# Kernel optimization log

Measured on AMD Instinct MI355X. Metric: run time of the kernel, lower is better.

## Reference

```python
import jax, jax.numpy as jnp
import numpy as np

B, F, D, U = 4096, 32, 64, 256


def setup_inputs() -> dict:
    key = jax.random.key(0)
    k1, k2, k3, k4 = jax.random.split(key, 4)
    embeds = jax.random.normal(k1, (B, F, D), dtype=jnp.float32)
    # glorot-ish scaling for the learned weights
    linear_w = jax.random.normal(k2, (F * D, U), dtype=jnp.float32) * (2.0 / (F * D + U)) ** 0.5
    inner_w = jax.random.normal(k3, (U, F), dtype=jnp.float32) * (2.0 / (U + F)) ** 0.5
    outer_w = jax.random.normal(k4, (U, D, D), dtype=jnp.float32) * (2.0 / (2 * D)) ** 0.5
    return {"embeds": embeds, "linear_w": linear_w, "inner_w": inner_w, "outer_w": outer_w}


def reference(embeds, linear_w, inner_w, outer_w):
    b = embeds.shape[0]
    # linear signal lz: flatten fields and project -> [B, U]
    lz = embeds.reshape(b, -1) @ linear_w
    # inner products: per unit u, delta_u = sum_f w_{u,f} * e_f  -> [B, U, D];
    # lp_inner[b,u] = ||delta_u||^2 (collapses the per-unit TF loop into one einsum)
    delta = jnp.einsum('bfd,uf->bud', embeds, inner_w)
    lp_inner = jnp.sum(jnp.square(delta), axis=2)  # [B, U]
    # outer products: product = fs fs^T with fs = sum_f e_f; lp_outer[b,u] = <product_b, W_u>
    fs = jnp.sum(embeds, axis=1)  # [B, D]
    lp_outer = jnp.einsum('bi,bj,uij->bu', fs, fs, outer_w)  # [B, U]
    return jnp.concatenate([lz, lp_inner, lp_outer], axis=1)  # [B, 3U]
```

## Files before the change

### kernel.cpp

```cpp
#include <hip/hip_runtime.h>
#include <hip/hip_bf16.h>


#define KA 3072
#define KW 7168

typedef __attribute__((ext_vector_type(8))) short short8v;
typedef __attribute__((ext_vector_type(4))) float f32x4;

#define GLOAD(src, dst) __builtin_amdgcn_global_load_lds( \
    (const __attribute__((address_space(1))) void*)(src), \
    (__attribute__((address_space(3))) void*)(dst), 16, 0, 0)

static __device__ __forceinline__ short f2bf(float f) {
    union { float f; unsigned u; } v; v.f = f;
    unsigned r = v.u + 0x7fffu + ((v.u >> 16) & 1u);
    return (short)(r >> 16);
}
static __device__ __forceinline__ float bf2f(short s) {
    union { unsigned u; float f; } v; v.u = ((unsigned)(unsigned short)s) << 16;
    return v.f;
}
static __device__ __forceinline__ int cvtpk(float lo, float hi) {
    int r;
    asm("v_cvt_pk_bf16_f32 %0, %1, %2" : "=v"(r) : "v"(lo), "v"(hi));
    return r;
}

__global__ __launch_bounds__(256) void prep(const float* __restrict__ embeds,
                                            const float* __restrict__ lw,
                                            const float* __restrict__ iw,
                                            const float* __restrict__ ow,
                                            short* __restrict__ A,
                                            short* __restrict__ FS,
                                            short* __restrict__ Wt) {
    __shared__ float se[2048];
    __shared__ short sebf[2048];
    int t = threadIdx.x;

    if (blockIdx.x < 4096) {
        int b = blockIdx.x;
        const float* e = embeds + (size_t)b * 2048;
        short* arow = A + (size_t)b * KA;

        float4 v0 = ((const float4*)e)[t * 2];
        float4 v1 = ((const float4*)e)[t * 2 + 1];
        ((float4*)se)[t * 2] = v0;
        ((float4*)se)[t * 2 + 1] = v1;
        short8v sb;
        sb[0] = f2bf(v0.x); sb[1] = f2bf(v0.y); sb[2] = f2bf(v0.z); sb[3] = f2bf(v0.w);
        sb[4] = f2bf(v1.x); sb[5] = f2bf(v1.y); sb[6] = f2bf(v1.z); sb[7] = f2bf(v1.w);
        ((short8v*)sebf)[t] = sb;
        *(short8v*)&arow[t * 8] = sb;

        __syncthreads();
        if (t < 64) {
            float s = 0.f;
            #pragma unroll
            for (int f = 0; f < 32; ++f) s += se[f * 64 + t];
            FS[(size_t)b * 64 + t] = f2bf(s);
        }

        int wid = t >> 6, lane = t & 63;
        int tm = wid >> 1, tn = wid & 1;
        int lr = lane & 15, lk = (lane >> 4) * 8;
        f32x4 g = {0.f, 0.f, 0.f, 0.f};
        #pragma unroll
        for (int ks = 0; ks < 2; ++ks) {
            short8v a  = *(const short8v*)&sebf[(tm * 16 + lr) * 64 + ks * 32 + lk];
            short8v bb = *(const short8v*)&sebf[(tn * 16 + lr) * 64 + ks * 32 + lk];
            g = __builtin_amdgcn_mfma_f32_16x16x32_bf16(a, bb, g, 0, 0, 0);
        }
        #pragma unroll
        for (int r = 0; r < 4; ++r) {
            int grow = tm * 16 + (lane >> 4) * 4 + r;
            int gcol = tn * 16 + lr;
            arow[2048 + grow * 32 + gcol] = f2bf(g[r]);
        }
    } else {
        int u = blockIdx.x - 4096;
        short* w = Wt + (size_t)u * KW;

        for (int k = t; k < 2048; k += 256) w[k] = f2bf(lw[(size_t)k * 256 + u]);

        if (t < 32) se[t] = iw[u * 32 + t];
        __syncthreads();
        for (int idx = t; idx < 1024; idx += 256)
            w[2048 + idx] = f2bf(se[idx >> 5] * se[idx & 31]);

        const float* owu = ow + (size_t)u * 4096;
        for (int i = t; i < 512; i += 256) {
            float4 a = ((const float4*)owu)[i * 2];
            float4 b = ((const float4*)owu)[i * 2 + 1];
            short8v s;
            s[0] = f2bf(a.x); s[1] = f2bf(a.y); s[2] = f2bf(a.z); s[3] = f2bf(a.w);
            s[4] = f2bf(b.x); s[5] = f2bf(b.y); s[6] = f2bf(b.z); s[7] = f2bf(b.w);
            *(short8v*)&w[3072 + i * 8] = s;
        }
    }
}

__global__ __launch_bounds__(256) void gemm_tile(const short* __restrict__ A,
                                                 const short* __restrict__ Wt,
                                                 const short* __restrict__ FS,
                                                 float* __restrict__ out) {
    __shared__ short As[2][8192];
    __shared__ short Bs[2][4096];

    int id = blockIdx.x;
    int seg, loc;
    if (id < 128)      { seg = 0; loc = id; }
    else if (id < 256) { seg = 2; loc = id - 128; }
    else               { seg = 1; loc = id - 256; }
    int mt = loc >> 2, nt = loc & 3;
    const int nk = (seg == 0) ? 32 : (seg == 1) ? 16 : 64;
    int brow = mt * 128, bcol = nt * 64;
    int akoff = (seg == 1) ? 2048 : 0;
    int boff  = (seg == 0) ? 0 : (seg == 1) ? 2048 : 3072;

    int t = threadIdx.x, w = t >> 6, lane = t & 63;
    int lr = lane & 15, hi = lane >> 4;
    int srow = t >> 3;
    int soct = (t & 7) ^ (srow & 7);

    const short* Asrc = A  + (size_t)(brow + srow) * KA + akoff + soct * 8;
    const short* Bsrc = Wt + (size_t)(bcol + srow) * KW + boff  + soct * 8;
    const short* Fsrc = FS + (size_t)(brow + srow) * 64 + soct * 8;

    auto stageA = [&](int p, int kt) {
        #pragma unroll
        for (int i = 0; i < 4; ++i)
            GLOAD(Asrc + (size_t)i * 32 * KA + kt * 64, &As[p][i * 2048 + t * 8]);
    };
    auto stageB = [&](int p, int kt) {
        #pragma unroll
        for (int i = 0; i < 2; ++i)
            GLOAD(Bsrc + (size_t)i * 32 * KW + kt * 64, &Bs[p][i * 2048 + t * 8]);
    };

    f32x4 acc[2][4];
    #pragma unroll
    for (int m = 0; m < 2; ++m)
        #pragma unroll
        for (int n = 0; n < 4; ++n) acc[m][n] = (f32x4){0.f, 0.f, 0.f, 0.f};

    if (seg == 2) {
        #pragma unroll
        for (int i = 0; i < 4; ++i)
            GLOAD(Fsrc + (size_t)i * 32 * 64, &As[0][i * 2048 + t * 8]);
        stageB(0, 0);
    } else {
        stageA(0, 0); stageB(0, 0);
    }
    __syncthreads();

    if (seg != 2) {
        for (int kt = 0; kt < nk; ++kt) {
            int cur = kt & 1;
            if (kt + 1 < nk) { stageA(cur ^ 1, kt + 1); stageB(cur ^ 1, kt + 1); }
            #pragma unroll
            for (int ks = 0; ks < 2; ++ks) {
                int oct = ((ks * 4 + hi) ^ (lr & 7)) * 8;
                short8v a[2], b[4];
                #pragma unroll
                for (int m = 0; m < 2; ++m)
                    a[m] = *(const short8v*)&As[cur][(w * 32 + m * 16 + lr) * 64 + oct];
                #pragma unroll
                for (int n = 0; n < 4; ++n)
                    b[n] = *(const short8v*)&Bs[cur][(n * 16 + lr) * 64 + oct];
                #pragma unroll
                for (int m = 0; m < 2; ++m)
                    #pragma unroll
                    for (int n = 0; n < 4; ++n)
                        acc[m][n] = __builtin_amdgcn_mfma_f32_16x16x32_bf16(a[m], b[n], acc[m][n], 0, 0, 0);
            }
            __syncthreads();
        }
    } else {
        float fj[2][2][8];
        #pragma unroll
        for (int m = 0; m < 2; ++m)
            #pragma unroll
            for (int ks = 0; ks < 2; ++ks) {
                int oct = ((ks * 4 + hi) ^ (lr & 7)) * 8;
                short8v v = *(const short8v*)&As[0][(w * 32 + m * 16 + lr) * 64 + oct];
                #pragma unroll
                for (int e = 0; e < 8; ++e) fj[m][ks][e] = bf2f(v[e]);
            }
        for (int kt = 0; kt < 64; ++kt) {
            int cur = kt & 1;
            if (kt + 1 < 64) stageB(cur ^ 1, kt + 1);
            int ioff = ((kt >> 3) ^ (lr & 7)) * 8 + (kt & 7);
            float s[2];
            #pragma unroll
            for (int m = 0; m < 2; ++m)
                s[m] = bf2f(As[0][(w * 32 + m * 16 + lr) * 64 + ioff]);
            #pragma unroll
            for (int ks = 0; ks < 2; ++ks) {
                int oct = ((ks * 4 + hi) ^ (lr & 7)) * 8;
                short8v b[4];
                #pragma unroll
                for (int n = 0; n < 4; ++n)
                    b[n] = *(const short8v*)&Bs[cur][(n * 16 + lr) * 64 + oct];
                #pragma unroll
                for (int m = 0; m < 2; ++m) {
                    union { int i32[4]; short8v v; } fa;
                    #pragma unroll
                    for (int q = 0; q < 4; ++q)
                        fa.i32[q] = cvtpk(s[m] * fj[m][ks][2 * q], s[m] * fj[m][ks][2 * q + 1]);
                    #pragma unroll
                    for (int n = 0; n < 4; ++n)
                        acc[m][n] = __builtin_amdgcn_mfma_f32_16x16x32_bf16(fa.v, b[n], acc[m][n], 0, 0, 0);
                }
            }
            __syncthreads();
        }
    }

    int segbase = seg * 256;
    #pragma unroll
    for (int m = 0; m < 2; ++m) {
        int row0 = brow + w * 32 + m * 16 + hi * 4;
        #pragma unroll
        for (int n = 0; n < 4; ++n) {
            int col = segbase + bcol + n * 16 + lr;
            #pragma unroll
            for (int r = 0; r < 4; ++r)
                out[(size_t)(row0 + r) * 768 + col] = acc[m][n][r];
        }
    }
}

extern "C" void kernel_launch(void* const* d_in, const int* in_sizes, int n_in,
                              void* d_out, int out_size, void* d_ws, size_t ws_size,
                              hipStream_t stream) {
    const float* embeds = (const float*)d_in[0];
    const float* lw = (const float*)d_in[1];
    const float* iw = (const float*)d_in[2];
    const float* ow = (const float*)d_in[3];
    float* out = (float*)d_out;

    short* A  = (short*)d_ws;
    short* Wt = A + (size_t)4096 * KA;
    short* FS = Wt + (size_t)256 * KW;

    prep<<<dim3(4352), dim3(256), 0, stream>>>(embeds, lw, iw, ow, A, FS, Wt);
    gemm_tile<<<dim3(384), dim3(256), 0, stream>>>(A, Wt, FS, out);
}
```

Before: 65.83 us.

## Triple-buffer LDS tiles with explicit vmcnt waits and XCD-aware block mapping

Replaces the double-buffered LDS pipeline with a three-stage ring, where loads run three K-tiles ahead and partial s_waitcnt vmcnt waits replace full __syncthreads. Block IDs are remapped so consecutive M tiles share an XCD, which should improve L2 reuse of A and B. MFMA sections are wrapped in s_setprio to favour the matrix issue. The cost is 1.5x the LDS per block, which may reduce occupancy. The hand-counted vmcnt values must match the number of outstanding global_load_lds ops or data races occur.

Measured after the change: 64.63 us. No clear change (-1.8%).

```diff
diff --git a/kernel.cpp b/kernel.cpp
--- a/kernel.cpp
+++ b/kernel.cpp
@@ -104,15 +104,13 @@
                                                  const short* __restrict__ Wt,
                                                  const short* __restrict__ FS,
                                                  float* __restrict__ out) {
-    __shared__ short As[2][8192];
-    __shared__ short Bs[2][4096];
+    __shared__ short As[3][8192];
+    __shared__ short Bs[3][4096];
 
     int id = blockIdx.x;
-    int seg, loc;
-    if (id < 128)      { seg = 0; loc = id; }
-    else if (id < 256) { seg = 2; loc = id - 128; }
-    else               { seg = 1; loc = id - 256; }
-    int mt = loc >> 2, nt = loc & 3;
+    int xcd = id & 7, slot = id >> 3, sgrp = slot >> 4, q = slot & 15;
+    int seg = (sgrp == 0) ? 2 : (sgrp == 1) ? 0 : 1;
+    int mt = xcd * 4 + (q >> 2), nt = q & 3;
     const int nk = (seg == 0) ? 32 : (seg == 1) ? 16 : 64;
     int brow = mt * 128, bcol = nt * 64;
     int akoff = (seg == 1) ? 2048 : 0;
@@ -144,39 +142,54 @@
         #pragma unroll
         for (int n = 0; n < 4; ++n) acc[m][n] = (f32x4){0.f, 0.f, 0.f, 0.f};
 
-    if (seg == 2) {
+    auto compute = [&](const short* a_s, const short* b_s) {
+        #pragma unroll
+        for (int ks = 0; ks < 2; ++ks) {
+            int oct = ((ks * 4 + hi) ^ (lr & 7)) * 8;
+            short8v a[2], b[4];
+            #pragma unroll
+            for (int m = 0; m < 2; ++m)
+                a[m] = *(const short8v*)&a_s[(w * 32 + m * 16 + lr) * 64 + oct];
+            #pragma unroll
+            for (int n = 0; n < 4; ++n)
+                b[n] = *(const short8v*)&b_s[(n * 16 + lr) * 64 + oct];
+            __builtin_amdgcn_s_setprio(1);
+            #pragma unroll
+            for (int m = 0; m < 2; ++m)
+                #pragma unroll
+                for (int n = 0; n < 4; ++n)
+                    acc[m][n] = __builtin_amdgcn_mfma_f32_16x16x32_bf16(a[m], b[n], acc[m][n], 0, 0, 0);
+            __builtin_amdgcn_s_setprio(0);
+        }
+    };
+
+    if (seg != 2) {
+        stageA(0, 0); stageB(0, 0);
+        stageA(1, 1); stageB(1, 1);
+        stageA(2, 2); stageB(2, 2);
+        __builtin_amdgcn_sched_barrier(0);
+        for (int kt = 0; kt < nk; ++kt) {
+            int cur = kt % 3;
+            if (kt + 2 < nk)      asm volatile("s_waitcnt vmcnt(12)" ::: "memory");
+            else if (kt + 1 < nk) asm volatile("s_waitcnt vmcnt(6)" ::: "memory");
+            else                  asm volatile("s_waitcnt vmcnt(0)" ::: "memory");
+            __builtin_amdgcn_s_barrier();
+            __builtin_amdgcn_sched_barrier(0);
+            compute(As[cur], Bs[cur]);
+            __builtin_amdgcn_sched_barrier(0);
+            __builtin_amdgcn_s_barrier();
+            if (kt + 3 < nk) { stageA(cur, kt + 3); stageB(cur, kt + 3); }
+            __builtin_amdgcn_sched_barrier(0);
+        }
+    } else {
         #pragma unroll
         for (int i = 0; i < 4; ++i)
             GLOAD(Fsrc + (size_t)i * 32 * 64, &As[0][i * 2048 + t * 8]);
-        stageB(0, 0);
-    } else {
-        stageA(0, 0); stageB(0, 0);
-    }
-    __syncthreads();
-
-    if (seg != 2) {
-        for (int kt = 0; kt < nk; ++kt) {
-            int cur = kt & 1;
-            if (kt + 1 < nk) { stageA(cur ^ 1, kt + 1); stageB(cur ^ 1, kt + 1); }
-            #pragma unroll
-            for (int ks = 0; ks < 2; ++ks) {
-                int oct = ((ks * 4 + hi) ^ (lr & 7)) * 8;
-                short8v a[2], b[4];
-                #pragma unroll
-                for (int m = 0; m < 2; ++m)
-                    a[m] = *(const short8v*)&As[cur][(w * 32 + m * 16 + lr) * 64 + oct];
-                #pragma unroll
-                for (int n = 0; n < 4; ++n)
-                    b[n] = *(const short8v*)&Bs[cur][(n * 16 + lr) * 64 + oct];
-                #pragma unroll
-                for (int m = 0; m < 2; ++m)
-                    #pragma unroll
-                    for (int n = 0; n < 4; ++n)
-                        acc[m][n] = __builtin_amdgcn_mfma_f32_16x16x32_bf16(a[m], b[n], acc[m][n], 0, 0, 0);
-            }
-            __syncthreads();
-        }
-    } else {
+        stageB(0, 0); stageB(1, 1); stageB(2, 2);
+        asm volatile("s_waitcnt vmcnt(6)" ::: "memory");
+        __builtin_amdgcn_s_barrier();
+        __builtin_amdgcn_sched_barrier(0);
+
         float fj[2][2][8];
         #pragma unroll
         for (int m = 0; m < 2; ++m)
@@ -188,8 +201,12 @@
                 for (int e = 0; e < 8; ++e) fj[m][ks][e] = bf2f(v[e]);
             }
         for (int kt = 0; kt < 64; ++kt) {
-            int cur = kt & 1;
-            if (kt + 1 < 64) stageB(cur ^ 1, kt + 1);
+            int cur = kt % 3;
+            if (kt + 2 < 64)      asm volatile("s_waitcnt vmcnt(4)" ::: "memory");
+            else if (kt + 1 < 64) asm volatile("s_waitcnt vmcnt(2)" ::: "memory");
+            else                  asm volatile("s_waitcnt vmcnt(0)" ::: "memory");
+            __builtin_amdgcn_s_barrier();
+            __builtin_amdgcn_sched_barrier(0);
             int ioff = ((kt >> 3) ^ (lr & 7)) * 8 + (kt & 7);
             float s[2];
             #pragma unroll
@@ -206,14 +223,19 @@
                 for (int m = 0; m < 2; ++m) {
                     union { int i32[4]; short8v v; } fa;
                     #pragma unroll
-                    for (int q = 0; q < 4; ++q)
-                        fa.i32[q] = cvtpk(s[m] * fj[m][ks][2 * q], s[m] * fj[m][ks][2 * q + 1]);
+                    for (int q2 = 0; q2 < 4; ++q2)
+                        fa.i32[q2] = cvtpk(s[m] * fj[m][ks][2 * q2], s[m] * fj[m][ks][2 * q2 + 1]);
+                    __builtin_amdgcn_s_setprio(1);
                     #pragma unroll
                     for (int n = 0; n < 4; ++n)
                         acc[m][n] = __builtin_amdgcn_mfma_f32_16x16x32_bf16(fa.v, b[n], acc[m][n], 0, 0, 0);
+                    __builtin_amdgcn_s_setprio(0);
                 }
             }
-            __syncthreads();
+            __builtin_amdgcn_sched_barrier(0);
+            __builtin_amdgcn_s_barrier();
+            if (kt + 3 < 64) stageB(cur, kt + 3);
+            __builtin_amdgcn_sched_barrier(0);
         }
     }
 
```

## Use 256x256 split-K tiles with atomic accumulation and on-the-fly outer-product generation

Applied to the files above, without the earlier changes.

Each GEMM block now covers a 256x256 output tile with 512 threads, and the K dimension is split into chunks so that 224 equally sized blocks do the work instead of 384 uneven ones. Partial sums are combined with float atomics into an output that a new kernel zeroes first. The outer-product segment now builds the fs_i*fs_j A tile into LDS in the background, interleaved with MFMA phases that use explicit barriers and s_setprio. This aims to balance load and improve reuse, at the cost of atomic traffic, an extra zeroing launch and higher register and LDS pressure.

Measured after the change: 99.16 us. 1.51x slower.

```diff
diff --git a/kernel.cpp b/kernel.cpp
--- a/kernel.cpp
+++ b/kernel.cpp
@@ -25,6 +25,13 @@
     int r;
     asm("v_cvt_pk_bf16_f32 %0, %1, %2" : "=v"(r) : "v"(lo), "v"(hi));
     return r;
+}
+
+__global__ __launch_bounds__(256) void zero_out(float4* __restrict__ out) {
+    size_t i = (size_t)blockIdx.x * 256 + threadIdx.x;
+    #pragma unroll
+    for (int r = 0; r < 3; ++r)
+        out[i + (size_t)r * 262144] = (float4){0.f, 0.f, 0.f, 0.f};
 }
 
 __global__ __launch_bounds__(256) void prep(const float* __restrict__ embeds,
@@ -100,133 +107,139 @@
     }
 }
 
-__global__ __launch_bounds__(256) void gemm_tile(const short* __restrict__ A,
-                                                 const short* __restrict__ Wt,
-                                                 const short* __restrict__ FS,
-                                                 float* __restrict__ out) {
-    __shared__ short As[2][8192];
-    __shared__ short Bs[2][4096];
+#define PHASE(CUR, KS, H, RB, LAST) do {                                            \
+    int oct_ = (((KS) * 4 + hi) ^ (lr & 7)) * 8;                                    \
+    short8v a_[4];                                                                  \
+    _Pragma("unroll")                                                               \
+    for (int m = 0; m < 4; ++m)                                                     \
+        a_[m] = *(const short8v*)&As[CUR][(wm * 128 + ((H) * 4 + m) * 16 + lr) * 64 + oct_]; \
+    if (RB) {                                                                       \
+        _Pragma("unroll")                                                           \
+        for (int n = 0; n < 4; ++n)                                                 \
+            bfr[n] = *(const short8v*)&Bs[CUR][(wn * 64 + n * 16 + lr) * 64 + oct_];\
+    }                                                                               \
+    __builtin_amdgcn_s_barrier();                                                   \
+    asm volatile("s_waitcnt lgkmcnt(0)" ::: "memory");                              \
+    __builtin_amdgcn_sched_barrier(0);                                              \
+    __builtin_amdgcn_s_setprio(1);                                                  \
+    _Pragma("unroll")                                                               \
+    for (int m = 0; m < 4; ++m)                                                     \
+        _Pragma("unroll")                                                           \
+        for (int n = 0; n < 4; ++n)                                                 \
+            acc[(H) * 4 + m][n] = __builtin_amdgcn_mfma_f32_16x16x32_bf16(a_[m], bfr[n], acc[(H) * 4 + m][n], 0, 0, 0); \
+    __builtin_amdgcn_s_setprio(0);                                                  \
+    if (LAST) asm volatile("s_waitcnt vmcnt(0)" ::: "memory");                      \
+    __builtin_amdgcn_s_barrier();                                                   \
+} while (0)
+
+#define GEN(BUF, P, SVAL) do {                                                      \
+    short8v fj_ = fsj[P];                                                           \
+    union { int i32[4]; short8v v; } g_;                                            \
+    _Pragma("unroll")                                                               \
+    for (int q = 0; q < 4; ++q)                                                     \
+        g_.i32[q] = cvtpk((SVAL) * bf2f(fj_[2 * q]), (SVAL) * bf2f(fj_[2 * q + 1]));\
+    int jo_ = ((P) + jhalf * 4) ^ (grow & 7);                                       \
+    *(short8v*)&As[BUF][grow * 64 + jo_ * 8] = g_.v;                                \
+} while (0)
+
+__global__ __launch_bounds__(512, 2) void gemm_tile(const short* __restrict__ A,
+                                                    const short* __restrict__ Wt,
+                                                    const short* __restrict__ FS,
+                                                    float* __restrict__ out) {
+    __shared__ short As[2][16384];
+    __shared__ short Bs[2][16384];
 
     int id = blockIdx.x;
-    int seg, loc;
-    if (id < 128)      { seg = 0; loc = id; }
-    else if (id < 256) { seg = 2; loc = id - 128; }
-    else               { seg = 1; loc = id - 256; }
-    int mt = loc >> 2, nt = loc & 3;
-    const int nk = (seg == 0) ? 32 : (seg == 1) ? 16 : 64;
-    int brow = mt * 128, bcol = nt * 64;
-    int akoff = (seg == 1) ? 2048 : 0;
-    int boff  = (seg == 0) ? 0 : (seg == 1) ? 2048 : 3072;
-
-    int t = threadIdx.x, w = t >> 6, lane = t & 63;
+    int mt = id / 14, c = id % 14;
+    int seg, kc;
+    if (c < 4)      { seg = 0; kc = c; }
+    else if (c < 6) { seg = 1; kc = c - 4; }
+    else            { seg = 2; kc = c - 6; }
+    int brow  = mt * 256;
+    int akoff = (seg == 0) ? kc * 512 : 2048 + kc * 512;
+    int boff  = (seg == 0) ? kc * 512 : (seg == 1) ? 2048 + kc * 512 : 3072 + kc * 512;
+
+    int t = threadIdx.x, wid = t >> 6, lane = t & 63;
+    int wm = wid >> 2, wn = wid & 3;
     int lr = lane & 15, hi = lane >> 4;
     int srow = t >> 3;
     int soct = (t & 7) ^ (srow & 7);
 
     const short* Asrc = A  + (size_t)(brow + srow) * KA + akoff + soct * 8;
-    const short* Bsrc = Wt + (size_t)(bcol + srow) * KW + boff  + soct * 8;
-    const short* Fsrc = FS + (size_t)(brow + srow) * 64 + soct * 8;
+    const short* Bsrc = Wt + (size_t)srow * KW + boff + soct * 8;
 
     auto stageA = [&](int p, int kt) {
         #pragma unroll
         for (int i = 0; i < 4; ++i)
-            GLOAD(Asrc + (size_t)i * 32 * KA + kt * 64, &As[p][i * 2048 + t * 8]);
+            GLOAD(Asrc + (size_t)i * 64 * KA + kt * 64, &As[p][i * 4096 + t * 8]);
     };
     auto stageB = [&](int p, int kt) {
         #pragma unroll
-        for (int i = 0; i < 2; ++i)
-            GLOAD(Bsrc + (size_t)i * 32 * KW + kt * 64, &Bs[p][i * 2048 + t * 8]);
+        for (int i = 0; i < 4; ++i)
+            GLOAD(Bsrc + (size_t)i * 64 * KW + kt * 64, &Bs[p][i * 4096 + t * 8]);
     };
 
-    f32x4 acc[2][4];
+    f32x4 acc[8][4];
     #pragma unroll
-    for (int m = 0; m < 2; ++m)
+    for (int m = 0; m < 8; ++m)
         #pragma unroll
         for (int n = 0; n < 4; ++n) acc[m][n] = (f32x4){0.f, 0.f, 0.f, 0.f};
-
-    if (seg == 2) {
-        #pragma unroll
-        for (int i = 0; i < 4; ++i)
-            GLOAD(Fsrc + (size_t)i * 32 * 64, &As[0][i * 2048 + t * 8]);
+    short8v bfr[4];
+
+    if (seg != 2) {
+        stageA(0, 0); stageB(0, 0);
+        __syncthreads();
+        for (int kt = 0; kt < 8; ++kt) {
+            int cur = kt & 1, nxt = cur ^ 1;
+            bool st = kt < 7;
+            if (st) stageA(nxt, kt + 1);
+            PHASE(cur, 0, 0, true, false);
+            if (st) stageB(nxt, kt + 1);
+            PHASE(cur, 0, 1, false, false);
+            PHASE(cur, 1, 0, true, false);
+            PHASE(cur, 1, 1, false, true);
+        }
+    } else {
+        int grow = t >> 1, jhalf = t & 1;
+        const short* fsrow = FS + (size_t)(brow + grow) * 64;
+        short8v fsi = *(const short8v*)(fsrow + kc * 8);
+        short8v fsj[4];
+        #pragma unroll
+        for (int q = 0; q < 4; ++q)
+            fsj[q] = *(const short8v*)(fsrow + jhalf * 32 + q * 8);
+
         stageB(0, 0);
-    } else {
-        stageA(0, 0); stageB(0, 0);
-    }
-    __syncthreads();
-
-    if (seg != 2) {
-        for (int kt = 0; kt < nk; ++kt) {
-            int cur = kt & 1;
-            if (kt + 1 < nk) { stageA(cur ^ 1, kt + 1); stageB(cur ^ 1, kt + 1); }
-            #pragma unroll
-            for (int ks = 0; ks < 2; ++ks) {
-                int oct = ((ks * 4 + hi) ^ (lr & 7)) * 8;
-                short8v a[2], b[4];
-                #pragma unroll
-                for (int m = 0; m < 2; ++m)
-                    a[m] = *(const short8v*)&As[cur][(w * 32 + m * 16 + lr) * 64 + oct];
-                #pragma unroll
-                for (int n = 0; n < 4; ++n)
-                    b[n] = *(const short8v*)&Bs[cur][(n * 16 + lr) * 64 + oct];
-                #pragma unroll
-                for (int m = 0; m < 2; ++m)
-                    #pragma unroll
-                    for (int n = 0; n < 4; ++n)
-                        acc[m][n] = __builtin_amdgcn_mfma_f32_16x16x32_bf16(a[m], b[n], acc[m][n], 0, 0, 0);
-            }
-            __syncthreads();
-        }
-    } else {
-        float fj[2][2][8];
-        #pragma unroll
-        for (int m = 0; m < 2; ++m)
-            #pragma unroll
-            for (int ks = 0; ks < 2; ++ks) {
-                int oct = ((ks * 4 + hi) ^ (lr & 7)) * 8;
-                short8v v = *(const short8v*)&As[0][(w * 32 + m * 16 + lr) * 64 + oct];
-                #pragma unroll
-                for (int e = 0; e < 8; ++e) fj[m][ks][e] = bf2f(v[e]);
-            }
-        for (int kt = 0; kt < 64; ++kt) {
-            int cur = kt & 1;
-            if (kt + 1 < 64) stageB(cur ^ 1, kt + 1);
-            int ioff = ((kt >> 3) ^ (lr & 7)) * 8 + (kt & 7);
-            float s[2];
-            #pragma unroll
-            for (int m = 0; m < 2; ++m)
-                s[m] = bf2f(As[0][(w * 32 + m * 16 + lr) * 64 + ioff]);
-            #pragma unroll
-            for (int ks = 0; ks < 2; ++ks) {
-                int oct = ((ks * 4 + hi) ^ (lr & 7)) * 8;
-                short8v b[4];
-                #pragma unroll
-                for (int n = 0; n < 4; ++n)
-                    b[n] = *(const short8v*)&Bs[cur][(n * 16 + lr) * 64 + oct];
-                #pragma unroll
-                for (int m = 0; m < 2; ++m) {
-                    union { int i32[4]; short8v v; } fa;
-                    #pragma unroll
-                    for (int q = 0; q < 4; ++q)
-                        fa.i32[q] = cvtpk(s[m] * fj[m][ks][2 * q], s[m] * fj[m][ks][2 * q + 1]);
-                    #pragma unroll
-                    for (int n = 0; n < 4; ++n)
-                        acc[m][n] = __builtin_amdgcn_mfma_f32_16x16x32_bf16(fa.v, b[n], acc[m][n], 0, 0, 0);
-                }
-            }
-            __syncthreads();
+        {
+            float s0 = bf2f(fsi[0]);
+            GEN(0, 0, s0); GEN(0, 1, s0); GEN(0, 2, s0); GEN(0, 3, s0);
+        }
+        __syncthreads();
+        #pragma unroll
+        for (int kt = 0; kt < 8; ++kt) {
+            int cur = kt & 1, nxt = cur ^ 1;
+            if (kt < 7) stageB(nxt, kt + 1);
+            float sn = (kt < 7) ? bf2f(fsi[(kt + 1) & 7]) : 0.f;
+            if (kt < 7) GEN(nxt, 0, sn);
+            PHASE(cur, 0, 0, true, false);
+            if (kt < 7) GEN(nxt, 1, sn);
+            PHASE(cur, 0, 1, false, false);
+            if (kt < 7) GEN(nxt, 2, sn);
+            PHASE(cur, 1, 0, true, false);
+            if (kt < 7) GEN(nxt, 3, sn);
+            PHASE(cur, 1, 1, false, true);
         }
     }
 
     int segbase = seg * 256;
     #pragma unroll
-    for (int m = 0; m < 2; ++m) {
-        int row0 = brow + w * 32 + m * 16 + hi * 4;
+    for (int m = 0; m < 8; ++m) {
+        int row0 = brow + wm * 128 + m * 16 + hi * 4;
         #pragma unroll
         for (int n = 0; n < 4; ++n) {
-            int col = segbase + bcol + n * 16 + lr;
+            int col = segbase + wn * 64 + n * 16 + lr;
             #pragma unroll
             for (int r = 0; r < 4; ++r)
-                out[(size_t)(row0 + r) * 768 + col] = acc[m][n][r];
+                unsafeAtomicAdd(&out[(size_t)(row0 + r) * 768 + col], acc[m][n][r]);
         }
     }
 }
@@ -244,6 +257,7 @@
     short* Wt = A + (size_t)4096 * KA;
     short* FS = Wt + (size_t)256 * KW;
 
+    zero_out<<<dim3(1024), dim3(256), 0, stream>>>((float4*)out);
     prep<<<dim3(4352), dim3(256), 0, stream>>>(embeds, lw, iw, ow, A, FS, Wt);
-    gemm_tile<<<dim3(384), dim3(256), 0, stream>>>(A, Wt, FS, out);
-}
+    gemm_tile<<<dim3(224), dim3(512), 0, stream>>>(A, Wt, FS, out);
+}
```
